# Kernel optimization log

Hardware: AMD Instinct MI355X
Metric: run time of the kernel (lower is better)

The kernel has to match this reference:

```python
import jax, jax.numpy as jnp
import numpy as np
import math

D_MODEL = 1024
NUM_HEADS = 16
D_K = D_MODEL // NUM_HEADS
SEQ_LEN = 2048
THETA = 10000.0


def _rope_tables(seq_len, d_k, theta):
    # inv_freq over even dims, angles repeated-interleaved to full d_k
    inv_freq = theta ** (-jnp.arange(0, d_k, 2, dtype=jnp.float32) / d_k)  # [d_k/2]
    pos = jnp.arange(seq_len, dtype=jnp.float32)                          # [s]
    angles = pos[:, None] * inv_freq[None, :]                             # [s, d_k/2]
    angles = jnp.repeat(angles, 2, axis=-1)                               # [s, d_k]
    return jnp.cos(angles), jnp.sin(angles)


def _rotate_half(x):
    # interleaved pairs: (x0,x1,x2,x3,...) -> (-x1,x0,-x3,x2,...)
    x_even = x[..., ::2]
    x_odd = x[..., 1::2]
    return jnp.stack([-x_odd, x_even], axis=-1).reshape(x.shape)


def _apply_rope(x, cos, sin):
    # x: [b, h, s, d_k]; cos/sin: [s, d_k]
    return x * cos + _rotate_half(x) * sin


def setup_inputs() -> dict:
    key = jax.random.key(0)
    ks = jax.random.split(key, 5)
    scale = 1.0 / math.sqrt(D_MODEL)
    X = jax.random.normal(ks[0], (2, SEQ_LEN, D_MODEL), dtype=jnp.float32)
    Wq = jax.random.normal(ks[1], (D_MODEL, D_MODEL), dtype=jnp.float32) * scale
    Wk = jax.random.normal(ks[2], (D_MODEL, D_MODEL), dtype=jnp.float32) * scale
    Wv = jax.random.normal(ks[3], (D_MODEL, D_MODEL), dtype=jnp.float32) * scale
    Wo = jax.random.normal(ks[4], (D_MODEL, D_MODEL), dtype=jnp.float32) * scale
    return {"X": X, "Wq": Wq, "Wk": Wk, "Wv": Wv, "Wo": Wo}


def reference(X, Wq, Wk, Wv, Wo):
    b, s, _ = X.shape
    h, dk = NUM_HEADS, D_K

    def proj(W):
        return (X @ W.T).reshape(b, s, h, dk).transpose(0, 2, 1, 3)  # [b,h,s,dk]

    q, k, v = proj(Wq), proj(Wk), proj(Wv)

    cos, sin = _rope_tables(s, dk, THETA)
    q = _apply_rope(q, cos, sin)
    k = _apply_rope(k, cos, sin)

    scores = jnp.einsum('bhid,bhjd->bhij', q, k) / math.sqrt(dk)
    causal = jnp.tril(jnp.ones((s, s), dtype=bool))
    scores = jnp.where(causal[None, None], scores, -jnp.inf)
    probs = jax.nn.softmax(scores, axis=-1)
    attended = jnp.einsum('bhij,bhjd->bhid', probs, v)               # [b,h,s,dk]

    out = attended.transpose(0, 2, 1, 3).reshape(b, s, h * dk)
    return out @ Wo.T
```

## Files before the change

kernel.cpp:

```cpp
#include <hip/hip_runtime.h>
#include <stdint.h>

#define D_MODEL 1024
#define NUM_HEADS 16
#define DK 64
#define SEQ 2048
#define BATCH 2
#define MROWS (BATCH * SEQ)
#define LOG2E 1.4426950408889634f
#define FIXM 14.0f

typedef short bf16x8 __attribute__((ext_vector_type(8)));
typedef float f32x4 __attribute__((ext_vector_type(4)));

__device__ __forceinline__ unsigned short f2bf(float f) {
    unsigned int u = __float_as_uint(f);
    u = (u + 0x7fffu + ((u >> 16) & 1u)) >> 16;
    return (unsigned short)u;
}
__device__ __forceinline__ unsigned short f2bf_trunc(float f) {
    return (unsigned short)(__float_as_uint(f) >> 16);
}
__device__ __forceinline__ float bf2f(unsigned short h) {
    return __uint_as_float(((unsigned int)h) << 16);
}
__device__ __forceinline__ void async16(const void* g, void* l) {
    __builtin_amdgcn_global_load_lds(
        (const __attribute__((address_space(1))) void*)g,
        (__attribute__((address_space(3))) void*)l, 16, 0, 0);
}
#define SWZ64(row, b) ((((row) * 8) + ((b) ^ ((row) & 7))) * 8)

__global__ void cast_all(const float4* __restrict__ X, const float4* __restrict__ Wq,
                         const float4* __restrict__ Wk, const float4* __restrict__ Wv,
                         const float4* __restrict__ Wo, ushort4* __restrict__ Xb,
                         ushort4* __restrict__ Wqkvb, ushort4* __restrict__ Wob,
                         float2* __restrict__ RT) {
    const int bx = blockIdx.x, t = threadIdx.x;
    if (bx < 8192) {
        int i = bx * 256 + t;
        const float4* src;
        ushort4* dst;
        int off;
        if (i < 1048576) { src = X; dst = Xb; off = i; }
        else if (i < 1310720) { src = Wq; dst = Wqkvb; off = i - 1048576; }
        else if (i < 1572864) { src = Wk; dst = Wqkvb + 262144; off = i - 1310720; }
        else if (i < 1835008) { src = Wv; dst = Wqkvb + 524288; off = i - 1572864; }
        else { src = Wo; dst = Wob; off = i - 1835008; }
        float4 v = src[off];
        ushort4 o;
        o.x = f2bf(v.x); o.y = f2bf(v.y); o.z = f2bf(v.z); o.w = f2bf(v.w);
        dst[off] = o;
    } else {
        int idx = (bx - 8192) * 256 + t;
        int f = idx >> 9;
        int s4 = (idx & 511) * 4;
        float invf = __expf(-(float)(2 * f) * (9.210340371976184f / 64.0f));
#pragma unroll
        for (int j = 0; j < 4; ++j) {
            int s = s4 + j;
            float sn, cs;
            __sincosf((float)s * invf, &sn, &cs);
            RT[f * SEQ + s] = make_float2(cs, sn);
        }
    }
}

template <int SWAP>
__global__ __launch_bounds__(256) void gemm_qkv(
    const unsigned short* __restrict__ A, const unsigned short* __restrict__ B,
    const float2* __restrict__ RT, unsigned short* __restrict__ Qr,
    unsigned short* __restrict__ Kr, unsigned short* __restrict__ Vt,
    int n_base) {
    __shared__ unsigned short As[128 * 64];
    __shared__ unsigned short Bs[128 * 64];
    const int K = D_MODEL;
    const int m0 = blockIdx.y * 128, n0 = n_base + blockIdx.x * 128;
    const int t = threadIdx.x;
    const int lane = t & 63, wave = t >> 6;
    const int mA = lane & 15, quad = lane >> 4;
    const int wr = (wave >> 1) * 64, wc = (wave & 1) * 64;

    f32x4 acc[4][4] = {};
    for (int k0 = 0; k0 < K; k0 += 64) {
#pragma unroll
        for (int i = 0; i < 4; ++i) {
            int ch = i * 256 + t;
            int r = ch >> 3, b = (ch & 7) ^ (r & 7);
            async16(A + (size_t)(m0 + r) * K + k0 + b * 8, (char*)As + ch * 16);
            async16(B + (size_t)(n0 + r) * K + k0 + b * 8, (char*)Bs + ch * 16);
        }
        __syncthreads();
#pragma unroll
        for (int kk = 0; kk < 2; ++kk) {
            bf16x8 af[4], bfr[4];
#pragma unroll
            for (int mi = 0; mi < 4; ++mi) {
                int rr = wr + mi * 16 + mA;
                af[mi] = *(const bf16x8*)&As[SWZ64(rr, kk * 4 + quad)];
            }
#pragma unroll
            for (int ni = 0; ni < 4; ++ni) {
                int rr = wc + ni * 16 + mA;
                bfr[ni] = *(const bf16x8*)&Bs[SWZ64(rr, kk * 4 + quad)];
            }
#pragma unroll
            for (int mi = 0; mi < 4; ++mi)
#pragma unroll
                for (int ni = 0; ni < 4; ++ni) {
                    if (SWAP)
                        acc[mi][ni] = __builtin_amdgcn_mfma_f32_16x16x32_bf16(
                            bfr[ni], af[mi], acc[mi][ni], 0, 0, 0);
                    else
                        acc[mi][ni] = __builtin_amdgcn_mfma_f32_16x16x32_bf16(
                            af[mi], bfr[ni], acc[mi][ni], 0, 0, 0);
                }
        }
        __syncthreads();
    }

    if (!SWAP) {
#pragma unroll
        for (int mi = 0; mi < 4; ++mi)
#pragma unroll
            for (int ni = 0; ni < 4; ++ni) {
                int gm = m0 + wr + mi * 16 + quad * 4;
                int gn = n0 + wc + ni * 16 + mA;
                int d = gn & 1023, h = d >> 6, dk = d & 63;
                int b = gm >> 11, s = gm & 2047;
                ushort4 o;
                o.x = f2bf(acc[mi][ni][0]);
                o.y = f2bf(acc[mi][ni][1]);
                o.z = f2bf(acc[mi][ni][2]);
                o.w = f2bf(acc[mi][ni][3]);
                *(ushort4*)&Vt[((size_t)(b * NUM_HEADS + h) * DK + dk) * SEQ + s] = o;
            }
    } else {
        unsigned short* Dst = (n0 >> 10) == 0 ? Qr : Kr;
#pragma unroll
        for (int mi = 0; mi < 4; ++mi) {
            int gm = m0 + wr + mi * 16 + mA;
            int b = gm >> 11, s = gm & 2047;
#pragma unroll
            for (int ni = 0; ni < 4; ++ni) {
                int gnb = n0 + wc + ni * 16 + quad * 4;
                int h = (gnb >> 6) & 15, dkb = gnb & 63;
                int f0 = dkb >> 1;
                float2 t0 = RT[f0 * SEQ + s];
                float2 t1 = RT[(f0 + 1) * SEQ + s];
                float a0 = acc[mi][ni][0], a1 = acc[mi][ni][1];
                float a2 = acc[mi][ni][2], a3 = acc[mi][ni][3];
                ushort4 o;
                o.x = f2bf(a0 * t0.x - a1 * t0.y);
                o.y = f2bf(a1 * t0.x + a0 * t0.y);
                o.z = f2bf(a2 * t1.x - a3 * t1.y);
                o.w = f2bf(a3 * t1.x + a2 * t1.y);
                *(ushort4*)&Dst[((size_t)(b * NUM_HEADS + h) * SEQ + s) * DK + dkb] = o;
            }
        }
    }
}

template <int TN, int OUT_BF16>
__global__ __launch_bounds__(256) void gemm_tile(
    const unsigned short* __restrict__ A, const unsigned short* __restrict__ B,
    void* __restrict__ Cout, int M, int N, int K) {
    __shared__ unsigned short As[128 * 64];
    __shared__ unsigned short Bs[TN * 64];
    const int m0 = blockIdx.y * 128, n0 = blockIdx.x * TN;
    const int t = threadIdx.x;
    const int lane = t & 63, wave = t >> 6;
    const int mA = lane & 15, quad = lane >> 4;
    constexpr int MI = (TN == 128) ? 4 : 2;
    constexpr int NI = 4;
    const int wr = (TN == 128) ? (wave >> 1) * 64 : wave * 32;
    const int wc = (TN == 128) ? (wave & 1) * 64 : 0;

    f32x4 acc[MI][NI] = {};
    for (int k0 = 0; k0 < K; k0 += 64) {
#pragma unroll
        for (int i = 0; i < 4; ++i) {
            int ch = i * 256 + t;
            int r = ch >> 3, b = (ch & 7) ^ (r & 7);
            async16(A + (size_t)(m0 + r) * K + k0 + b * 8, (char*)As + ch * 16);
        }
#pragma unroll
        for (int i = 0; i < TN / 32; ++i) {
            int ch = i * 256 + t;
            int r = ch >> 3, b = (ch & 7) ^ (r & 7);
            async16(B + (size_t)(n0 + r) * K + k0 + b * 8, (char*)Bs + ch * 16);
        }
        __syncthreads();
#pragma unroll
        for (int kk = 0; kk < 2; ++kk) {
            bf16x8 af[MI], bfr[NI];
#pragma unroll
            for (int mi = 0; mi < MI; ++mi) {
                int rr = wr + mi * 16 + mA;
                af[mi] = *(const bf16x8*)&As[SWZ64(rr, kk * 4 + quad)];
            }
#pragma unroll
            for (int ni = 0; ni < NI; ++ni) {
                int rr = wc + ni * 16 + mA;
                bfr[ni] = *(const bf16x8*)&Bs[SWZ64(rr, kk * 4 + quad)];
            }
#pragma unroll
            for (int mi = 0; mi < MI; ++mi)
#pragma unroll
                for (int ni = 0; ni < NI; ++ni)
                    acc[mi][ni] = __builtin_amdgcn_mfma_f32_16x16x32_bf16(
                        af[mi], bfr[ni], acc[mi][ni], 0, 0, 0);
        }
        __syncthreads();
    }
#pragma unroll
    for (int mi = 0; mi < MI; ++mi)
#pragma unroll
        for (int ni = 0; ni < NI; ++ni)
#pragma unroll
            for (int r = 0; r < 4; ++r) {
                int gm = m0 + wr + mi * 16 + quad * 4 + r;
                int gn = n0 + wc + ni * 16 + mA;
                if (OUT_BF16)
                    ((unsigned short*)Cout)[(size_t)gm * N + gn] = f2bf(acc[mi][ni][r]);
                else
                    ((float*)Cout)[(size_t)gm * N + gn] = acc[mi][ni][r];
            }
}

__global__ __launch_bounds__(256, 4) void flash_attn6(
    const unsigned short* __restrict__ Qr, const unsigned short* __restrict__ Kr,
    const unsigned short* __restrict__ Vt, unsigned short* __restrict__ Att) {
    __shared__ unsigned short Ks[2][64 * 64];
    __shared__ unsigned short Vs[2][64 * 64];
    __shared__ unsigned short Ps[4][16 * 64];
    const int bh = blockIdx.x;
    const int qt = 31 - (int)blockIdx.y;
    const int t = threadIdx.x;
    const int lane = t & 63, wave = t >> 6;
    const int mA = lane & 15, quad = lane >> 4;
    const int qr0 = qt * 64 + wave * 16;
    const size_t qkbase = (size_t)bh * SEQ * DK;
    const unsigned short* Kg = Kr + qkbase;
    const unsigned short* Vg = Vt + (size_t)bh * DK * SEQ;

    bf16x8 aq[2];
#pragma unroll
    for (int c = 0; c < 2; ++c) {
        bf16x8 raw = *(const bf16x8*)&Qr[qkbase + (size_t)(qr0 + mA) * DK + c * 32 + quad * 8];
        bf16x8 s;
#pragma unroll
        for (int j = 0; j < 8; ++j)
            s[j] = (short)f2bf(bf2f((unsigned short)raw[j]) * (0.125f * LOG2E));
        aq[c] = s;
    }

    f32x4 accT[4] = {};
    float lsum[4] = {};

#pragma unroll
    for (int i = 0; i < 2; ++i) {
        int ch = i * 256 + t;
        int row = ch >> 3, sb = (ch & 7) ^ (row & 7);
        async16(Kg + (size_t)row * DK + sb * 8, (char*)Ks[0] + ch * 16);
        async16(Vg + (size_t)row * SEQ + sb * 8, (char*)Vs[0] + ch * 16);
    }

    for (int jt = 0; jt <= qt; ++jt) {
        __syncthreads();
        const int cur = jt & 1;
        if (jt < qt) {
            const int j1 = (jt + 1) * 64;
#pragma unroll
            for (int i = 0; i < 2; ++i) {
                int ch = i * 256 + t;
                int row = ch >> 3, sb = (ch & 7) ^ (row & 7);
                async16(Kg + (size_t)(j1 + row) * DK + sb * 8, (char*)Ks[cur ^ 1] + ch * 16);
                async16(Vg + (size_t)row * SEQ + j1 + sb * 8, (char*)Vs[cur ^ 1] + ch * 16);
            }
        }
        const int j0 = jt * 64;
        const unsigned short* Kt = Ks[cur];
        const unsigned short* Vtile = Vs[cur];
        unsigned short* Pw = Ps[wave];

        f32x4 sc[4] = {};
#pragma unroll
        for (int js = 0; js < 4; ++js) {
            int row = js * 16 + mA;
            bf16x8 b0 = *(const bf16x8*)&Kt[SWZ64(row, quad)];
            bf16x8 b1 = *(const bf16x8*)&Kt[SWZ64(row, quad + 4)];
            sc[js] = __builtin_amdgcn_mfma_f32_16x16x32_bf16(aq[0], b0, sc[js], 0, 0, 0);
            sc[js] = __builtin_amdgcn_mfma_f32_16x16x32_bf16(aq[1], b1, sc[js], 0, 0, 0);
        }
        if (jt == qt) {
#pragma unroll
            for (int js = 0; js < 4; ++js) {
                int gcol = j0 + js * 16 + mA;
#pragma unroll
                for (int r = 0; r < 4; ++r)
                    if (gcol > qr0 + quad * 4 + r) sc[js][r] = -1e30f;
            }
        }

#pragma unroll
        for (int js = 0; js < 4; ++js)
#pragma unroll
            for (int r = 0; r < 4; ++r) {
                float p = __builtin_amdgcn_exp2f(sc[js][r] - FIXM);
                lsum[r] += p;
                int q = quad * 4 + r;
                Pw[SWZ64(q, js * 2 + (mA >> 3)) + (mA & 7)] = f2bf_trunc(p);
            }
        bf16x8 ap0 = *(const bf16x8*)&Pw[SWZ64(mA, quad)];
        bf16x8 ap1 = *(const bf16x8*)&Pw[SWZ64(mA, quad + 4)];
#pragma unroll
        for (int tn = 0; tn < 4; ++tn) {
            int row = tn * 16 + mA;
            bf16x8 bv0 = *(const bf16x8*)&Vtile[SWZ64(row, quad)];
            bf16x8 bv1 = *(const bf16x8*)&Vtile[SWZ64(row, quad + 4)];
            accT[tn] = __builtin_amdgcn_mfma_f32_16x16x32_bf16(bv0, ap0, accT[tn], 0, 0, 0);
            accT[tn] = __builtin_amdgcn_mfma_f32_16x16x32_bf16(bv1, ap1, accT[tn], 0, 0, 0);
        }
    }

#pragma unroll
    for (int r = 0; r < 4; ++r)
#pragma unroll
        for (int off = 1; off < 16; off <<= 1)
            lsum[r] += __shfl_xor(lsum[r], off, 64);
    __syncthreads();
    float* LL = (float*)Ks;
    if (mA == 0)
#pragma unroll
        for (int r = 0; r < 4; ++r) LL[wave * 16 + quad * 4 + r] = lsum[r];
    __syncthreads();
    const float rl = 1.0f / LL[wave * 16 + mA];

    const int b = bh >> 4, h = bh & 15;
#pragma unroll
    for (int tn = 0; tn < 4; ++tn) {
        ushort4 o;
        o.x = f2bf(accT[tn][0] * rl);
        o.y = f2bf(accT[tn][1] * rl);
        o.z = f2bf(accT[tn][2] * rl);
        o.w = f2bf(accT[tn][3] * rl);
        *(ushort4*)&Att[(size_t)(b * SEQ + qr0 + mA) * D_MODEL + h * DK + tn * 16 + quad * 4] = o;
    }
}

extern "C" void kernel_launch(void* const* d_in, const int* in_sizes, int n_in,
                              void* d_out, int out_size, void* d_ws, size_t ws_size,
                              hipStream_t stream) {
    const float* X = (const float*)d_in[0];
    const float* Wq = (const float*)d_in[1];
    const float* Wk = (const float*)d_in[2];
    const float* Wv = (const float*)d_in[3];
    const float* Wo = (const float*)d_in[4];

    char* ws = (char*)d_ws;
    unsigned short* Xb    = (unsigned short*)(ws + 0);
    unsigned short* Wqkvb = (unsigned short*)(ws + (8u << 20));
    unsigned short* Wob   = (unsigned short*)(ws + (14u << 20));
    unsigned short* Qr    = (unsigned short*)(ws + (16u << 20));
    unsigned short* Kr    = (unsigned short*)(ws + (24u << 20));
    unsigned short* Vt    = (unsigned short*)(ws + (32u << 20));
    unsigned short* Att   = (unsigned short*)(ws + (40u << 20));
    float2*         RT    = (float2*)(ws + (48u << 20));

    cast_all<<<8192 + 64, 256, 0, stream>>>((const float4*)X, (const float4*)Wq,
                                            (const float4*)Wk, (const float4*)Wv,
                                            (const float4*)Wo, (ushort4*)Xb,
                                            (ushort4*)Wqkvb, (ushort4*)Wob, RT);

    gemm_qkv<1><<<dim3(16, MROWS / 128), 256, 0, stream>>>(
        Xb, Wqkvb, RT, Qr, Kr, Vt, 0);
    gemm_qkv<0><<<dim3(8, MROWS / 128), 256, 0, stream>>>(
        Xb, Wqkvb, RT, Qr, Kr, Vt, 2048);

    flash_attn6<<<dim3(BATCH * NUM_HEADS, 32), 256, 0, stream>>>(Qr, Kr, Vt, Att);

    gemm_tile<64, 0><<<dim3(D_MODEL / 64, MROWS / 128), 256, 0, stream>>>(
        Att, Wob, d_out, MROWS, D_MODEL, D_MODEL);
}
```

Measured before the change: 188.4 us.

## Merge QKV GEMM launches into one grid and widen output GEMM K-tile

The two templated QKV projection launches (Q/K with RoPE epilogue and V with transposed store) are merged into a single 24-column grid that branches on blockIdx.x. This removes one kernel launch and lets the V blocks run alongside the Q/K blocks so the GPU fills better. The output projection becomes a dedicated kernel with a 128-wide K step and a 128-column swizzle, which halves the number of barrier-synchronised iterations. The cost is more LDS per block (48KB), which may reduce occupancy.

```diff
diff --git a/kernel.cpp b/kernel.cpp
--- a/kernel.cpp
+++ b/kernel.cpp
@@ -30,6 +30,7 @@
         (__attribute__((address_space(3))) void*)l, 16, 0, 0);
 }
 #define SWZ64(row, b) ((((row) * 8) + ((b) ^ ((row) & 7))) * 8)
+#define SWZ128(row, b) ((((row) * 16) + ((b) ^ ((row) & 7))) * 8)
 
 __global__ void cast_all(const float4* __restrict__ X, const float4* __restrict__ Wq,
                          const float4* __restrict__ Wk, const float4* __restrict__ Wv,
@@ -66,77 +67,55 @@
     }
 }
 
-template <int SWAP>
 __global__ __launch_bounds__(256) void gemm_qkv(
     const unsigned short* __restrict__ A, const unsigned short* __restrict__ B,
     const float2* __restrict__ RT, unsigned short* __restrict__ Qr,
-    unsigned short* __restrict__ Kr, unsigned short* __restrict__ Vt,
-    int n_base) {
+    unsigned short* __restrict__ Kr, unsigned short* __restrict__ Vt) {
     __shared__ unsigned short As[128 * 64];
     __shared__ unsigned short Bs[128 * 64];
     const int K = D_MODEL;
-    const int m0 = blockIdx.y * 128, n0 = n_base + blockIdx.x * 128;
+    const int bx = blockIdx.x;
+    const int m0 = blockIdx.y * 128;
     const int t = threadIdx.x;
     const int lane = t & 63, wave = t >> 6;
     const int mA = lane & 15, quad = lane >> 4;
     const int wr = (wave >> 1) * 64, wc = (wave & 1) * 64;
 
-    f32x4 acc[4][4] = {};
-    for (int k0 = 0; k0 < K; k0 += 64) {
-#pragma unroll
-        for (int i = 0; i < 4; ++i) {
-            int ch = i * 256 + t;
-            int r = ch >> 3, b = (ch & 7) ^ (r & 7);
-            async16(A + (size_t)(m0 + r) * K + k0 + b * 8, (char*)As + ch * 16);
-            async16(B + (size_t)(n0 + r) * K + k0 + b * 8, (char*)Bs + ch * 16);
-        }
-        __syncthreads();
-#pragma unroll
-        for (int kk = 0; kk < 2; ++kk) {
-            bf16x8 af[4], bfr[4];
-#pragma unroll
-            for (int mi = 0; mi < 4; ++mi) {
-                int rr = wr + mi * 16 + mA;
-                af[mi] = *(const bf16x8*)&As[SWZ64(rr, kk * 4 + quad)];
-            }
-#pragma unroll
-            for (int ni = 0; ni < 4; ++ni) {
-                int rr = wc + ni * 16 + mA;
-                bfr[ni] = *(const bf16x8*)&Bs[SWZ64(rr, kk * 4 + quad)];
-            }
-#pragma unroll
-            for (int mi = 0; mi < 4; ++mi)
+    if (bx < 16) {
+        const int n0 = bx * 128;
+        f32x4 acc[4][4] = {};
+        for (int k0 = 0; k0 < K; k0 += 64) {
+#pragma unroll
+            for (int i = 0; i < 4; ++i) {
+                int ch = i * 256 + t;
+                int r = ch >> 3, b = (ch & 7) ^ (r & 7);
+                async16(A + (size_t)(m0 + r) * K + k0 + b * 8, (char*)As + ch * 16);
+                async16(B + (size_t)(n0 + r) * K + k0 + b * 8, (char*)Bs + ch * 16);
+            }
+            __syncthreads();
+#pragma unroll
+            for (int kk = 0; kk < 2; ++kk) {
+                bf16x8 af[4], bfr[4];
+#pragma unroll
+                for (int mi = 0; mi < 4; ++mi) {
+                    int rr = wr + mi * 16 + mA;
+                    af[mi] = *(const bf16x8*)&As[SWZ64(rr, kk * 4 + quad)];
+                }
 #pragma unroll
                 for (int ni = 0; ni < 4; ++ni) {
-                    if (SWAP)
+                    int rr = wc + ni * 16 + mA;
+                    bfr[ni] = *(const bf16x8*)&Bs[SWZ64(rr, kk * 4 + quad)];
+                }
+#pragma unroll
+                for (int mi = 0; mi < 4; ++mi)
+#pragma unroll
+                    for (int ni = 0; ni < 4; ++ni)
                         acc[mi][ni] = __builtin_amdgcn_mfma_f32_16x16x32_bf16(
                             bfr[ni], af[mi], acc[mi][ni], 0, 0, 0);
-                    else
-                        acc[mi][ni] = __builtin_amdgcn_mfma_f32_16x16x32_bf16(
-                            af[mi], bfr[ni], acc[mi][ni], 0, 0, 0);
-                }
-        }
-        __syncthreads();
-    }
-
-    if (!SWAP) {
-#pragma unroll
-        for (int mi = 0; mi < 4; ++mi)
-#pragma unroll
-            for (int ni = 0; ni < 4; ++ni) {
-                int gm = m0 + wr + mi * 16 + quad * 4;
-                int gn = n0 + wc + ni * 16 + mA;
-                int d = gn & 1023, h = d >> 6, dk = d & 63;
-                int b = gm >> 11, s = gm & 2047;
-                ushort4 o;
-                o.x = f2bf(acc[mi][ni][0]);
-                o.y = f2bf(acc[mi][ni][1]);
-                o.z = f2bf(acc[mi][ni][2]);
-                o.w = f2bf(acc[mi][ni][3]);
-                *(ushort4*)&Vt[((size_t)(b * NUM_HEADS + h) * DK + dk) * SEQ + s] = o;
-            }
-    } else {
-        unsigned short* Dst = (n0 >> 10) == 0 ? Qr : Kr;
+            }
+            __syncthreads();
+        }
+        unsigned short* Dst = (n0 < 1024) ? Qr : Kr;
 #pragma unroll
         for (int mi = 0; mi < 4; ++mi) {
             int gm = m0 + wr + mi * 16 + mA;
@@ -158,73 +137,117 @@
                 *(ushort4*)&Dst[((size_t)(b * NUM_HEADS + h) * SEQ + s) * DK + dkb] = o;
             }
         }
-    }
-}
-
-template <int TN, int OUT_BF16>
-__global__ __launch_bounds__(256) void gemm_tile(
+    } else {
+        const int n0 = 2048 + (bx - 16) * 128;
+        f32x4 acc[4][4] = {};
+        for (int k0 = 0; k0 < K; k0 += 64) {
+#pragma unroll
+            for (int i = 0; i < 4; ++i) {
+                int ch = i * 256 + t;
+                int r = ch >> 3, b = (ch & 7) ^ (r & 7);
+                async16(A + (size_t)(m0 + r) * K + k0 + b * 8, (char*)As + ch * 16);
+                async16(B + (size_t)(n0 + r) * K + k0 + b * 8, (char*)Bs + ch * 16);
+            }
+            __syncthreads();
+#pragma unroll
+            for (int kk = 0; kk < 2; ++kk) {
+                bf16x8 af[4], bfr[4];
+#pragma unroll
+                for (int mi = 0; mi < 4; ++mi) {
+                    int rr = wr + mi * 16 + mA;
+                    af[mi] = *(const bf16x8*)&As[SWZ64(rr, kk * 4 + quad)];
+                }
+#pragma unroll
+                for (int ni = 0; ni < 4; ++ni) {
+                    int rr = wc + ni * 16 + mA;
+                    bfr[ni] = *(const bf16x8*)&Bs[SWZ64(rr, kk * 4 + quad)];
+                }
+#pragma unroll
+                for (int mi = 0; mi < 4; ++mi)
+#pragma unroll
+                    for (int ni = 0; ni < 4; ++ni)
+                        acc[mi][ni] = __builtin_amdgcn_mfma_f32_16x16x32_bf16(
+                            af[mi], bfr[ni], acc[mi][ni], 0, 0, 0);
+            }
+            __syncthreads();
+        }
+#pragma unroll
+        for (int mi = 0; mi < 4; ++mi)
+#pragma unroll
+            for (int ni = 0; ni < 4; ++ni) {
+                int gm = m0 + wr + mi * 16 + quad * 4;
+                int gn = n0 + wc + ni * 16 + mA;
+                int d = gn & 1023, h = d >> 6, dk = d & 63;
+                int b = gm >> 11, s = gm & 2047;
+                ushort4 o;
+                o.x = f2bf(acc[mi][ni][0]);
+                o.y = f2bf(acc[mi][ni][1]);
+                o.z = f2bf(acc[mi][ni][2]);
+                o.w = f2bf(acc[mi][ni][3]);
+                *(ushort4*)&Vt[((size_t)(b * NUM_HEADS + h) * DK + dk) * SEQ + s] = o;
+            }
+    }
+}
+
+__global__ __launch_bounds__(256) void gemm_out(
     const unsigned short* __restrict__ A, const unsigned short* __restrict__ B,
-    void* __restrict__ Cout, int M, int N, int K) {
-    __shared__ unsigned short As[128 * 64];
-    __shared__ unsigned short Bs[TN * 64];
-    const int m0 = blockIdx.y * 128, n0 = blockIdx.x * TN;
+    float* __restrict__ Cout, int M, int N, int K) {
+    __shared__ unsigned short As[128 * 128];
+    __shared__ unsigned short Bs[64 * 128];
+    const int m0 = blockIdx.y * 128, n0 = blockIdx.x * 64;
     const int t = threadIdx.x;
     const int lane = t & 63, wave = t >> 6;
     const int mA = lane & 15, quad = lane >> 4;
-    constexpr int MI = (TN == 128) ? 4 : 2;
-    constexpr int NI = 4;
-    const int wr = (TN == 128) ? (wave >> 1) * 64 : wave * 32;
-    const int wc = (TN == 128) ? (wave & 1) * 64 : 0;
-
-    f32x4 acc[MI][NI] = {};
-    for (int k0 = 0; k0 < K; k0 += 64) {
+    const int wr = wave * 32;
+
+    f32x4 acc[2][4] = {};
+    for (int k0 = 0; k0 < K; k0 += 128) {
+#pragma unroll
+        for (int i = 0; i < 8; ++i) {
+            int ch = i * 256 + t;
+            int r = ch >> 4, bl = ch & 15;
+            int b = bl ^ (r & 7);
+            async16(A + (size_t)(m0 + r) * K + k0 + b * 8, (char*)As + ch * 16);
+        }
 #pragma unroll
         for (int i = 0; i < 4; ++i) {
             int ch = i * 256 + t;
-            int r = ch >> 3, b = (ch & 7) ^ (r & 7);
-            async16(A + (size_t)(m0 + r) * K + k0 + b * 8, (char*)As + ch * 16);
-        }
-#pragma unroll
-        for (int i = 0; i < TN / 32; ++i) {
-            int ch = i * 256 + t;
-            int r = ch >> 3, b = (ch & 7) ^ (r & 7);
+            int r = ch >> 4, bl = ch & 15;
+            int b = bl ^ (r & 7);
             async16(B + (size_t)(n0 + r) * K + k0 + b * 8, (char*)Bs + ch * 16);
         }
         __syncthreads();
 #pragma unroll
-        for (int kk = 0; kk < 2; ++kk) {
-            bf16x8 af[MI], bfr[NI];
-#pragma unroll
-            for (int mi = 0; mi < MI; ++mi) {
+        for (int kk = 0; kk < 4; ++kk) {
+            bf16x8 af[2], bfr[4];
+#pragma unroll
+            for (int mi = 0; mi < 2; ++mi) {
                 int rr = wr + mi * 16 + mA;
-                af[mi] = *(const bf16x8*)&As[SWZ64(rr, kk * 4 + quad)];
-            }
-#pragma unroll
-            for (int ni = 0; ni < NI; ++ni) {
-                int rr = wc + ni * 16 + mA;
-                bfr[ni] = *(const bf16x8*)&Bs[SWZ64(rr, kk * 4 + quad)];
-            }
-#pragma unroll
-            for (int mi = 0; mi < MI; ++mi)
-#pragma unroll
-                for (int ni = 0; ni < NI; ++ni)
+                af[mi] = *(const bf16x8*)&As[SWZ128(rr, kk * 4 + quad)];
+            }
+#pragma unroll
+            for (int ni = 0; ni < 4; ++ni) {
+                int rr = ni * 16 + mA;
+                bfr[ni] = *(const bf16x8*)&Bs[SWZ128(rr, kk * 4 + quad)];
+            }
+#pragma unroll
+            for (int mi = 0; mi < 2; ++mi)
+#pragma unroll
+                for (int ni = 0; ni < 4; ++ni)
                     acc[mi][ni] = __builtin_amdgcn_mfma_f32_16x16x32_bf16(
                         af[mi], bfr[ni], acc[mi][ni], 0, 0, 0);
         }
         __syncthreads();
     }
 #pragma unroll
-    for (int mi = 0; mi < MI; ++mi)
-#pragma unroll
-        for (int ni = 0; ni < NI; ++ni)
+    for (int mi = 0; mi < 2; ++mi)
+#pragma unroll
+        for (int ni = 0; ni < 4; ++ni)
 #pragma unroll
             for (int r = 0; r < 4; ++r) {
                 int gm = m0 + wr + mi * 16 + quad * 4 + r;
-                int gn = n0 + wc + ni * 16 + mA;
-                if (OUT_BF16)
-                    ((unsigned short*)Cout)[(size_t)gm * N + gn] = f2bf(acc[mi][ni][r]);
-                else
-                    ((float*)Cout)[(size_t)gm * N + gn] = acc[mi][ni][r];
+                int gn = n0 + ni * 16 + mA;
+                Cout[(size_t)gm * N + gn] = acc[mi][ni][r];
             }
 }
 
@@ -373,13 +396,11 @@
                                             (const float4*)Wo, (ushort4*)Xb,
                                             (ushort4*)Wqkvb, (ushort4*)Wob, RT);
 
-    gemm_qkv<1><<<dim3(16, MROWS / 128), 256, 0, stream>>>(
-        Xb, Wqkvb, RT, Qr, Kr, Vt, 0);
-    gemm_qkv<0><<<dim3(8, MROWS / 128), 256, 0, stream>>>(
-        Xb, Wqkvb, RT, Qr, Kr, Vt, 2048);
+    gemm_qkv<<<dim3(24, MROWS / 128), 256, 0, stream>>>(
+        Xb, Wqkvb, RT, Qr, Kr, Vt);
 
     flash_attn6<<<dim3(BATCH * NUM_HEADS, 32), 256, 0, stream>>>(Qr, Kr, Vt, Att);
 
-    gemm_tile<64, 0><<<dim3(D_MODEL / 64, MROWS / 128), 256, 0, stream>>>(
-        Att, Wob, d_out, MROWS, D_MODEL, D_MODEL);
-}
+    gemm_out<<<dim3(D_MODEL / 64, MROWS / 128), 256, 0, stream>>>(
+        Att, Wob, (float*)d_out, MROWS, D_MODEL, D_MODEL);
+}
```

New measurement: 185.2 us. About the same (-1.7%).
